# Performance work log

Measured on AMD Instinct MI355X. Metric: run time of the kernel, lower is better.

## Reference

```python
import jax, jax.numpy as jnp
import numpy as np

V, E, H, G, L, T, B = 32000, 1024, 16, 4, 8, 1024, 2
NKV = H // G          # kv heads = 4
D = E // H            # head dim = 64
BLOCK = 1024          # block_size
EPS = 1e-5


def setup_inputs() -> dict:
    key = jax.random.key(0)
    ks = jax.random.split(key, 12)
    f32 = jnp.float32
    return {
        "idx": jax.random.randint(ks[0], (B, T), 0, V),
        "tok_emb": jax.random.normal(ks[1], (V, E), f32),
        "pos_emb": jax.random.normal(ks[2], (BLOCK, E), f32),
        "q_proj": jax.random.normal(ks[3], (L, E, G, NKV, D), f32) / E**0.5,
        "kv_proj": jax.random.normal(ks[4], (L, 2, E, NKV, D), f32) / E**0.5,
        "out_proj": jax.random.normal(ks[5], (L, E, E), f32) / (D * H)**0.5,
        "fc_in": jax.random.normal(ks[6], (L, E, 4 * E), f32) / E**0.5,
        "fc_out": jax.random.normal(ks[7], (L, 4 * E, E), f32) / (4 * E)**0.5,
        "scale": jnp.ones((L, 2, E), f32),
        "out_scale": jnp.ones((E,), f32),
        "lm_head": jax.random.normal(ks[8], (E, V), f32) / E**0.5,
    }


def _ln(x, w):
    mu = jnp.mean(x, axis=-1, keepdims=True)
    var = jnp.var(x, axis=-1, keepdims=True)
    return (x - mu) * jax.lax.rsqrt(var + EPS) * w


def reference(idx, tok_emb, pos_emb, q_proj, kv_proj, out_proj, fc_in, fc_out, scale, out_scale, lm_head):
    x = tok_emb[idx] + pos_emb[:T]                         # [B,T,E]
    causal = jnp.tril(jnp.ones((T, T), bool))              # [T,T]
    neg_inf = jnp.float32(-jnp.inf)

    def layer(x, params):
        w_kv, w_q, w_out, fc1, fc2, lscale = params
        h = _ln(x, lscale[0])                              # pre-LN (note: residual uses h, matching source)
        q = jnp.einsum('btc,cgnd->bgntd', h, w_q)          # [B,G,NKV,T,D]
        kv = jnp.einsum('btc,scnd->sbntd', h, w_kv)        # [2,B,NKV,T,D]
        k, v = kv[0], kv[1]
        att = jnp.einsum('bgnqd,bnkd->bgnqk', q, k) * (D ** -0.5)
        att = jnp.where(causal, att, neg_inf)
        att = jax.nn.softmax(att, axis=-1)
        o = jnp.einsum('bgnqk,bnkd->bgnqd', att, v)        # [B,G,NKV,T,D]
        o = jnp.transpose(o, (0, 3, 1, 2, 4)).reshape(B, T, E)
        o = jnp.einsum('btc,cd->btd', o, w_out)
        h = h + o
        h = _ln(h, lscale[1])
        mlp = jax.nn.relu(jnp.einsum('btc,cf->btf', h, fc1))
        mlp = jnp.einsum('btf,fc->btc', mlp, fc2)
        return h + mlp, None

    x, _ = jax.lax.scan(layer, x, (kv_proj, q_proj, out_proj, fc_in, fc_out, scale))
    x = _ln(x, out_scale)
    logits = jnp.einsum('btc,cv->btv', x, lm_head)         # [B,T,V]
    return logits
```

## Files before the change

### kernel.cpp

```cpp
#include <hip/hip_runtime.h>
#include <hip/hip_bf16.h>

typedef __attribute__((ext_vector_type(8))) short bf16x8;
typedef __attribute__((ext_vector_type(4))) short bf16x4;
typedef __attribute__((ext_vector_type(4))) float f32x4;

#define LB __launch_bounds__(256)

__device__ __forceinline__ unsigned short f2b(float f) {
  __hip_bfloat16 h = __float2bfloat16(f);
  return __builtin_bit_cast(unsigned short, h);
}

#define GLDS(gp, lp)                                                        \
  __builtin_amdgcn_global_load_lds(                                         \
      (const __attribute__((address_space(1))) void*)(gp),                  \
      (__attribute__((address_space(3))) void*)(lp), 16, 0, 0)

__global__ LB void embed_kernel(const int* __restrict__ idx, const float* __restrict__ tok,
                                const float* __restrict__ pos, float* __restrict__ X) {
  const int m = blockIdx.x;
  const int t = m & 1023;
  const int token = idx[m];
  const int c = threadIdx.x * 4;
  const float4 a = *(const float4*)(tok + (size_t)token * 1024 + c);
  const float4 p = *(const float4*)(pos + (size_t)t * 1024 + c);
  float4 o; o.x = a.x + p.x; o.y = a.y + p.y; o.z = a.z + p.z; o.w = a.w + p.w;
  *(float4*)(X + (size_t)m * 1024 + c) = o;
}

template<bool WF32>
__global__ LB void ln_kernel(const float* __restrict__ X, const float* __restrict__ W,
                             float* __restrict__ Yf, unsigned short* __restrict__ Yb) {
  const int row = blockIdx.x;
  const float* xr = X + (size_t)row * 1024;
  const int c = threadIdx.x * 4;
  const float4 v = *(const float4*)(xr + c);
  float s = v.x + v.y + v.z + v.w;
  float q = v.x*v.x + v.y*v.y + v.z*v.z + v.w*v.w;
  #pragma unroll
  for (int d = 32; d > 0; d >>= 1) { s += __shfl_down(s, d); q += __shfl_down(q, d); }
  __shared__ float ss[4], sq[4];
  const int wid = threadIdx.x >> 6;
  if ((threadIdx.x & 63) == 0) { ss[wid] = s; sq[wid] = q; }
  __syncthreads();
  const float fs = ss[0] + ss[1] + ss[2] + ss[3];
  const float fq = sq[0] + sq[1] + sq[2] + sq[3];
  const float mean = fs * (1.0f / 1024.0f);
  const float var = fq * (1.0f / 1024.0f) - mean * mean;
  const float rstd = rsqrtf(var + 1e-5f);
  const float4 w = *(const float4*)(W + c);
  float4 o;
  o.x = (v.x - mean) * rstd * w.x; o.y = (v.y - mean) * rstd * w.y;
  o.z = (v.z - mean) * rstd * w.z; o.w = (v.w - mean) * rstd * w.w;
  if (WF32) *(float4*)(Yf + (size_t)row * 1024 + c) = o;
  unsigned long long pk = (unsigned long long)f2b(o.x)
      | ((unsigned long long)f2b(o.y) << 16)
      | ((unsigned long long)f2b(o.z) << 32)
      | ((unsigned long long)f2b(o.w) << 48);
  *(unsigned long long*)(Yb + (size_t)row * 1024 + c) = pk;
}

__device__ __forceinline__ void tr_body(const float* __restrict__ src,
                                        unsigned short* __restrict__ dst,
                                        int C, int rowOff, int ldDst, int bx, int by) {
  __shared__ float tile[32][33];
  const int c0 = bx * 32, r0 = by * 32;
  const int tx = threadIdx.x & 31, ty = threadIdx.x >> 5;
  #pragma unroll
  for (int u = 0; u < 4; ++u)
    tile[ty + u * 8][tx] = src[(size_t)(r0 + ty + u * 8) * C + c0 + tx];
  __syncthreads();
  const int ci = threadIdx.x >> 4;
  const int rp = threadIdx.x & 15;
  #pragma unroll
  for (int u = 0; u < 2; ++u) {
    const int c = ci + u * 16;
    unsigned int pk = (unsigned int)f2b(tile[rp * 2][c])
                    | ((unsigned int)f2b(tile[rp * 2 + 1][c]) << 16);
    *(unsigned int*)&dst[(size_t)(rowOff + c0 + c) * ldDst + r0 + rp * 2] = pk;
  }
}

__global__ LB void transpose_w(const float* __restrict__ src, unsigned short* __restrict__ dst,
                               int C, int rowOff, int ldDst) {
  tr_body(src, dst, C, rowOff, ldDst, blockIdx.x, blockIdx.y);
}

__global__ LB void transpose_all(const float* __restrict__ qp, const float* __restrict__ op,
                                 const float* __restrict__ kvp, unsigned short* __restrict__ dstQ,
                                 const float* __restrict__ f1, const float* __restrict__ f2,
                                 unsigned short* __restrict__ F1T, unsigned short* __restrict__ F2T) {
  int id = blockIdx.x;
  if (id < 2560) {
    const float* src; int C, rowOff, bx, by;
    if (id < 2048) {
      src = (id < 1024) ? qp : op;
      rowOff = (id < 1024) ? 0 : 1536;
      id &= 1023; C = 1024; bx = id & 31; by = id >> 5;
    } else {
      id -= 2048;
      src = (id < 256) ? kvp : (kvp + 1024 * 256);
      rowOff = (id < 256) ? 1024 : 1280;
      id &= 255; C = 256; bx = id & 7; by = id >> 3;
    }
    tr_body(src, dstQ, C, rowOff, 1024, bx, by);
  } else {
    id -= 2560;
    if (id < 4096) {
      tr_body(f1, F1T, 4096, 0, 1024, id & 127, id >> 7);
    } else {
      id -= 4096;
      tr_body(f2, F2T, 1024, 0, 4096, id & 31, id >> 5);
    }
  }
}

__global__ LB void attn_fused(const unsigned short* __restrict__ qkvb,
                              const unsigned short* __restrict__ vT,
                              unsigned short* __restrict__ ob) {
  const int qt = 15 - blockIdx.x, bh = blockIdx.y;
  const int b = bh >> 4, hh = bh & 15, n = hh & 3;
  const int tid = threadIdx.x, lane = tid & 63, w = tid >> 6;
  const int g = lane >> 4, c = lane & 15;
  const int q0w = qt * 64 + w * 16;
  const int qrow = q0w + c;

  __shared__ unsigned short lsK[2][64 * 64];
  __shared__ unsigned short lsV[2][64 * 64];
  __shared__ unsigned short lsP[4][16 * 64];
  unsigned short* Pw = lsP[w];

  bf16x8 qf[2];
  {
    const unsigned short* Qb = qkvb + (size_t)(b * 1024 + q0w) * 1536 + hh * 64;
    #pragma unroll
    for (int ks = 0; ks < 2; ++ks)
      qf[ks] = *(const bf16x8*)(Qb + (size_t)c * 1536 + ks * 32 + g * 8);
  }

  f32x4 accO[4] = {};
  float mr = -1e30f, lr = 0.0f;

  const int srow = tid >> 3;
  const int scol = ((tid & 7) ^ (srow & 7)) << 3;
  const unsigned short* gK = qkvb + (size_t)(b * 1024 + srow) * 1536 + 1024 + n * 64 + scol;
  const unsigned short* gV = vT + (size_t)((b * 4 + n) * 64 + srow) * 1024 + scol;

  GLDS(gK, &lsK[0][tid * 8]);
  GLDS(gK + (size_t)32 * 1536, &lsK[0][tid * 8 + 2048]);
  GLDS(gV, &lsV[0][tid * 8]);
  GLDS(gV + (size_t)32 * 1024, &lsV[0][tid * 8 + 2048]);
  __syncthreads();

  for (int kt = 0; kt <= qt; ++kt) {
    const int cur = kt & 1;
    if (kt < qt) {
      const size_t ko = (size_t)(kt + 1) * 64;
      GLDS(gK + ko * 1536, &lsK[cur ^ 1][tid * 8]);
      GLDS(gK + (ko + 32) * 1536, &lsK[cur ^ 1][tid * 8 + 2048]);
      GLDS(gV + ko, &lsV[cur ^ 1][tid * 8]);
      GLDS(gV + ko + (size_t)32 * 1024, &lsV[cur ^ 1][tid * 8 + 2048]);
    }
    const unsigned short* K_ = lsK[cur];
    const unsigned short* V_ = lsV[cur];
    const bool dg = (kt == qt);
    const int kb = kt * 64;

    f32x4 st[4] = {};
    #pragma unroll
    for (int ks = 0; ks < 2; ++ks) {
      const int col = (((ks * 4 + g) ^ (lane & 7)) << 3);
      bf16x8 kf[4];
      #pragma unroll
      for (int mi = 0; mi < 4; ++mi)
        kf[mi] = *(const bf16x8*)&K_[(mi * 16 + c) * 64 + col];
      #pragma unroll
      for (int mi = 0; mi < 4; ++mi)
        st[mi] = __builtin_amdgcn_mfma_f32_16x16x32_bf16(kf[mi], qf[ks], st[mi], 0, 0, 0);
    }

    float mx = mr;
    #pragma unroll
    for (int mi = 0; mi < 4; ++mi)
      #pragma unroll
      for (int j = 0; j < 4; ++j) {
        float v = st[mi][j] * 0.125f;
        if (dg && (kb + mi * 16 + g * 4 + j) > qrow) v = -1e30f;
        st[mi][j] = v;
        mx = fmaxf(mx, v);
      }
    mx = fmaxf(mx, __shfl_xor(mx, 16));
    mx = fmaxf(mx, __shfl_xor(mx, 32));
    const float al = __expf(mr - mx);
    float sum = 0.0f;
    #pragma unroll
    for (int mi = 0; mi < 4; ++mi) {
      bf16x4 pk;
      #pragma unroll
      for (int j = 0; j < 4; ++j) {
        const float e = __expf(st[mi][j] - mx);
        sum += e;
        pk[j] = (short)f2b(e);
      }
      *(bf16x4*)&Pw[c * 64 + ((mi * 16 + g * 4) ^ ((c & 7) << 3))] = pk;
    }
    sum += __shfl_xor(sum, 16);
    sum += __shfl_xor(sum, 32);
    lr = lr * al + sum;
    mr = mx;

    float aj[4];
    #pragma unroll
    for (int j = 0; j < 4; ++j) aj[j] = __shfl(al, g * 4 + j);
    #pragma unroll
    for (int dj = 0; dj < 4; ++dj)
      #pragma unroll
      for (int j = 0; j < 4; ++j) accO[dj][j] *= aj[j];

    #pragma unroll
    for (int ks = 0; ks < 2; ++ks) {
      const int col = (((ks * 4 + g) ^ (c & 7)) << 3);
      const bf16x8 pa = *(const bf16x8*)&Pw[c * 64 + col];
      bf16x8 vf[4];
      #pragma unroll
      for (int dj = 0; dj < 4; ++dj)
        vf[dj] = *(const bf16x8*)&V_[(dj * 16 + c) * 64 + col];
      #pragma unroll
      for (int dj = 0; dj < 4; ++dj)
        accO[dj] = __builtin_amdgcn_mfma_f32_16x16x32_bf16(pa, vf[dj], accO[dj], 0, 0, 0);
    }
    __syncthreads();
  }

  const float linv = 1.0f / lr;
  float lj[4];
  #pragma unroll
  for (int j = 0; j < 4; ++j) lj[j] = __shfl(linv, g * 4 + j);
  unsigned short* obase = ob + (size_t)(b * 1024 + q0w) * 1024 + hh * 64;
  #pragma unroll
  for (int dj = 0; dj < 4; ++dj)
    #pragma unroll
    for (int j = 0; j < 4; ++j)
      obase[(size_t)(g * 4 + j) * 1024 + dj * 16 + c] = f2b(accO[dj][j] * lj[j]);
}

template<int BM, int BN, bool BF16OUT, bool RELU, bool RESID, bool WVT = false, bool DBUF = false>
__global__ LB void gemm_nt(const unsigned short* __restrict__ A, const unsigned short* __restrict__ Bt,
                           void* __restrict__ Cv, const float* __restrict__ Res,
                           unsigned short* __restrict__ vTo,
                           int K, int lda, int ldb, int ldc) {
  constexpr int BK = 64;
  constexpr int WM = BM / 2, WN = BN / 2;
  constexpr int FM = WM / 16, FN = WN / 16;
  constexpr int PA = BM / 32, PB = BN / 32;
  constexpr int NB = DBUF ? 2 : 1;
  int f = blockIdx.x + gridDim.x * blockIdx.y;
  const int nwg = gridDim.x * gridDim.y;
  if ((nwg & 7) == 0) f = (f & 7) * (nwg >> 3) + (f >> 3);
  const int bx = f % gridDim.x, by = f / gridDim.x;

  const int tid = threadIdx.x;
  const int lane = tid & 63, wid = tid >> 6;
  const int wr = wid >> 1, wc = wid & 1;
  const int m0 = bx * BM, n0 = by * BN;

  __shared__ unsigned short lsA[NB][BM * BK];
  __shared__ unsigned short lsB[NB][BN * BK];

  f32x4 acc[FM][FN] = {};

  const int srow = tid >> 3;
  const int scol = ((tid & 7) ^ (srow & 7)) << 3;
  const unsigned short* gA = A + (size_t)(m0 + srow) * lda + scol;
  const unsigned short* gB = Bt + (size_t)(n0 + srow) * ldb + scol;

  const int fr = lane & 15;
  const int j7 = lane & 7;
  const int g4 = lane >> 4;

  if (DBUF) {
    #pragma unroll
    for (int p = 0; p < PA; ++p) GLDS(gA + (size_t)(p * 32) * lda, &lsA[0][tid * 8 + p * 2048]);
    #pragma unroll
    for (int p = 0; p < PB; ++p) GLDS(gB + (size_t)(p * 32) * ldb, &lsB[0][tid * 8 + p * 2048]);
    __syncthreads();
  }

  for (int k0 = 0; k0 < K; k0 += BK) {
    int cur = 0;
    if (DBUF) {
      cur = (k0 >> 6) & 1;
      if (k0 + BK < K) {
        #pragma unroll
        for (int p = 0; p < PA; ++p)
          GLDS(gA + (size_t)(p * 32) * lda + k0 + BK, &lsA[cur ^ 1][tid * 8 + p * 2048]);
        #pragma unroll
        for (int p = 0; p < PB; ++p)
          GLDS(gB + (size_t)(p * 32) * ldb + k0 + BK, &lsB[cur ^ 1][tid * 8 + p * 2048]);
      }
    } else {
      if (k0) __syncthreads();
      #pragma unroll
      for (int p = 0; p < PA; ++p)
        GLDS(gA + (size_t)(p * 32) * lda + k0, &lsA[0][tid * 8 + p * 2048]);
      #pragma unroll
      for (int p = 0; p < PB; ++p)
        GLDS(gB + (size_t)(p * 32) * ldb + k0, &lsB[0][tid * 8 + p * 2048]);
      __syncthreads();
    }

    const unsigned short* LA = lsA[cur];
    const unsigned short* LBp = lsB[cur];
    #pragma unroll
    for (int ks = 0; ks < 2; ++ks) {
      const int col = (((ks * 4 + g4) ^ j7) << 3);
      bf16x8 af[FM], bfv[FN];
      #pragma unroll
      for (int mi = 0; mi < FM; ++mi)
        af[mi] = *(const bf16x8*)&LA[(wr * WM + mi * 16 + fr) * BK + col];
      #pragma unroll
      for (int nj = 0; nj < FN; ++nj)
        bfv[nj] = *(const bf16x8*)&LBp[(wc * WN + nj * 16 + fr) * BK + col];
      #pragma unroll
      for (int mi = 0; mi < FM; ++mi)
        #pragma unroll
        for (int nj = 0; nj < FN; ++nj)
          acc[mi][nj] = __builtin_amdgcn_mfma_f32_16x16x32_bf16(af[mi], bfv[nj], acc[mi][nj], 0, 0, 0);
    }
    if (DBUF) __syncthreads();
  }

  const int r0 = (lane >> 4) * 4, c0 = lane & 15;
  #pragma unroll
  for (int mi = 0; mi < FM; ++mi) {
    #pragma unroll
    for (int nj = 0; nj < FN; ++nj) {
      const int c = n0 + wc * WN + nj * 16 + c0;
      const int rb = m0 + wr * WM + mi * 16 + r0;
      unsigned short us[4];
      #pragma unroll
      for (int j = 0; j < 4; ++j) {
        const int r = rb + j;
        float v = acc[mi][nj][j];
        if (RELU) v = fmaxf(v, 0.0f);
        if (RESID) v += Res[(size_t)r * ldc + c];
        const size_t o = (size_t)r * ldc + c;
        if (BF16OUT) { us[j] = f2b(v); ((unsigned short*)Cv)[o] = us[j]; }
        else ((float*)Cv)[o] = v;
      }
      if (WVT && c >= 1280) {
        const int bb = rb >> 10, t0 = rb & 1023;
        bf16x4 pk;
        #pragma unroll
        for (int j = 0; j < 4; ++j) pk[j] = (short)us[j];
        *(bf16x4*)&vTo[((size_t)(bb * 256 + (c - 1280))) * 1024 + t0] = pk;
      }
    }
  }
}

extern "C" void kernel_launch(void* const* d_in, const int* in_sizes, int n_in,
                              void* d_out, int out_size, void* d_ws, size_t ws_size,
                              hipStream_t stream) {
  (void)in_sizes; (void)n_in; (void)out_size;
  const int*   idx      = (const int*)d_in[0];
  const float* tok_emb  = (const float*)d_in[1];
  const float* pos_emb  = (const float*)d_in[2];
  const float* q_proj   = (const float*)d_in[3];
  const float* kv_proj  = (const float*)d_in[4];
  const float* out_proj = (const float*)d_in[5];
  const float* fc_in    = (const float*)d_in[6];
  const float* fc_out   = (const float*)d_in[7];
  const float* scale    = (const float*)d_in[8];
  const float* out_scl  = (const float*)d_in[9];
  const float* lm_head  = (const float*)d_in[10];
  float* out = (float*)d_out;

  char* ws = (char*)d_ws;
  size_t off = 0;
  auto alloc = [&](size_t bytes) -> void* {
    void* p = ws + off;
    off += (bytes + 255) & ~(size_t)255;
    return p;
  };
  unsigned short* WqkvT = (unsigned short*)alloc((size_t)2560 * 1024 * 2);
  unsigned short* WoT   = WqkvT + (size_t)1536 * 1024;
  unsigned short* F1T   = (unsigned short*)alloc((size_t)4096 * 1024 * 2);
  unsigned short* F2T   = (unsigned short*)alloc((size_t)1024 * 4096 * 2);
  float*  xbuf  = (float*)alloc((size_t)2048 * 1024 * 4);
  float*  hbuf  = (float*)alloc((size_t)2048 * 1024 * 4);
  float*  h2buf = (float*)alloc((size_t)2048 * 1024 * 4);
  unsigned short* actb  = (unsigned short*)alloc((size_t)2048 * 1024 * 2);
  unsigned short* qkvb  = (unsigned short*)alloc((size_t)2048 * 1536 * 2);
  unsigned short* vT    = (unsigned short*)alloc((size_t)2 * 256 * 1024 * 2);
  unsigned short* LmT   = (unsigned short*)alloc((size_t)32000 * 1024 * 2);
  unsigned short* ob    = (unsigned short*)alloc((size_t)2048 * 1024 * 2);
  unsigned short* m1    = (unsigned short*)alloc((size_t)2048 * 4096 * 2);
  if (off > ws_size) return;

  const dim3 thr(256);

  embed_kernel<<<dim3(2048), thr, 0, stream>>>(idx, tok_emb, pos_emb, xbuf);

  for (int l = 0; l < 8; ++l) {
    const float* qp  = q_proj + (size_t)l * 1024 * 1024;
    const float* op  = out_proj + (size_t)l * 1024 * 1024;
    const float* kvp = kv_proj + (size_t)l * 2 * 1024 * 256;
    transpose_all<<<dim3(10752), thr, 0, stream>>>(
        qp, op, kvp, WqkvT,
        fc_in + (size_t)l * 1024 * 4096, fc_out + (size_t)l * 4096 * 1024, F1T, F2T);

    const float* w1 = scale + (size_t)l * 2048;
    const float* w2 = w1 + 1024;

    ln_kernel<true><<<dim3(2048), thr, 0, stream>>>(xbuf, w1, hbuf, actb);
    gemm_nt<128, 64, true, false, false, true, true><<<dim3(16, 24), thr, 0, stream>>>(
        actb, WqkvT, qkvb, nullptr, vT, 1024, 1024, 1024, 1536);
    attn_fused<<<dim3(16, 32), thr, 0, stream>>>(qkvb, vT, ob);
    gemm_nt<128, 64, false, false, true, false, true><<<dim3(16, 16), thr, 0, stream>>>(
        ob, WoT, xbuf, hbuf, nullptr, 1024, 1024, 1024, 1024);
    ln_kernel<true><<<dim3(2048), thr, 0, stream>>>(xbuf, w2, h2buf, actb);
    gemm_nt<128, 128, true, true, false, false, true><<<dim3(16, 32), thr, 0, stream>>>(
        actb, F1T, m1, nullptr, nullptr, 1024, 1024, 1024, 4096);
    gemm_nt<128, 64, false, false, true, false, true><<<dim3(16, 16), thr, 0, stream>>>(
        m1, F2T, xbuf, h2buf, nullptr, 4096, 4096, 4096, 1024);
  }

  transpose_w<<<dim3(1000, 32), thr, 0, stream>>>(lm_head, LmT, 32000, 0, 1024);
  ln_kernel<false><<<dim3(2048), thr, 0, stream>>>(xbuf, out_scl, nullptr, actb);
  gemm_nt<128, 128, false, false, false><<<dim3(16, 250), thr, 0, stream>>>(
      actb, LmT, out, nullptr, nullptr, 1024, 1024, 1024, 32000);
}
```

Measured before the change: 1.536 ms.

## Add 256x256 double-buffered 8-wave GEMM for the LM head projection

Replaces the 128x128 LM-head GEMM with a new 512-thread kernel that computes 256x256 output tiles. It double-buffers XOR-swizzled LDS tiles filled by direct global-to-LDS loads, issues the next tile's loads interleaved across four quadrant sub-steps, raises wave priority around the MFMA bursts, and remaps workgroup IDs for locality. The goal is more data reuse per loaded byte and better overlap of memory traffic with matrix math on the largest GEMM. In exchange it uses 128 KB of LDS and many accumulator registers, which limits occupancy, and it needs careful manual vmcnt and barrier ordering.

```diff
diff --git a/kernel.cpp b/kernel.cpp
--- a/kernel.cpp
+++ b/kernel.cpp
@@ -16,6 +16,9 @@
   __builtin_amdgcn_global_load_lds(                                         \
       (const __attribute__((address_space(1))) void*)(gp),                  \
       (__attribute__((address_space(3))) void*)(lp), 16, 0, 0)
+
+#define WAITV(n) asm volatile("s_waitcnt vmcnt(" #n ")" ::: "memory")
+#define SBAR() do { __builtin_amdgcn_s_barrier(); asm volatile("" ::: "memory"); } while (0)
 
 __global__ LB void embed_kernel(const int* __restrict__ idx, const float* __restrict__ tok,
                                 const float* __restrict__ pos, float* __restrict__ X) {
@@ -355,6 +358,112 @@
         #pragma unroll
         for (int j = 0; j < 4; ++j) pk[j] = (short)us[j];
         *(bf16x4*)&vTo[((size_t)(bb * 256 + (c - 1280))) * 1024 + t0] = pk;
+      }
+    }
+  }
+}
+
+__global__ __launch_bounds__(512) void gemm_big(const unsigned short* __restrict__ A,
+                                                const unsigned short* __restrict__ Bt,
+                                                float* __restrict__ C,
+                                                int K, int lda, int ldb, int ldc) {
+  int f = blockIdx.x + gridDim.x * blockIdx.y;
+  const int nwg = gridDim.x * gridDim.y;
+  f = (f & 7) * (nwg >> 3) + (f >> 3);
+  const int bx = f % gridDim.x, by = f / gridDim.x;
+  const int m0 = bx * 256, n0 = by * 256;
+
+  const int tid = threadIdx.x;
+  const int lane = tid & 63, wid = tid >> 6;
+  const int wr = wid >> 2, wc = wid & 3;
+  const int fr = lane & 15, g4 = lane >> 4, j7 = lane & 7;
+
+  __shared__ unsigned short lsA[2][256 * 64];
+  __shared__ unsigned short lsB[2][256 * 64];
+
+  f32x4 acc[8][4] = {};
+
+  const int srow = tid >> 3;
+  const int scol = ((tid & 7) ^ (srow & 7)) << 3;
+  const unsigned short* gA = A + (size_t)(m0 + srow) * lda + scol;
+  const unsigned short* gB = Bt + (size_t)(n0 + srow) * ldb + scol;
+
+  const int nt = K >> 6;
+
+  GLDS(gB + (size_t)(0 * 64) * ldb, &lsB[0][tid * 8 + 0 * 4096]);
+  GLDS(gB + (size_t)(1 * 64) * ldb, &lsB[0][tid * 8 + 1 * 4096]);
+  GLDS(gB + (size_t)(2 * 64) * ldb, &lsB[0][tid * 8 + 2 * 4096]);
+  GLDS(gB + (size_t)(3 * 64) * ldb, &lsB[0][tid * 8 + 3 * 4096]);
+  GLDS(gA + (size_t)(0 * 64) * lda, &lsA[0][tid * 8 + 0 * 4096]);
+  GLDS(gA + (size_t)(2 * 64) * lda, &lsA[0][tid * 8 + 2 * 4096]);
+  GLDS(gA + (size_t)(1 * 64) * lda, &lsA[0][tid * 8 + 1 * 4096]);
+  GLDS(gA + (size_t)(3 * 64) * lda, &lsA[0][tid * 8 + 3 * 4096]);
+
+  for (int t = 0; t < nt; ++t) {
+    const int cur = t & 1;
+    const bool pref = (t + 1) < nt;
+    const int k1 = (t + 1) << 6;
+    const unsigned short* TA = lsA[cur];
+    const unsigned short* TB = lsB[cur];
+    unsigned short* nA = &lsA[cur ^ 1][tid * 8];
+    unsigned short* nB = &lsB[cur ^ 1][tid * 8];
+
+    WAITV(2);
+    SBAR();
+
+    #pragma unroll
+    for (int q = 0; q < 4; ++q) {
+      const int qm = q >> 1, qn = q & 1;
+      bf16x8 af[2][4], bf[2][2];
+      #pragma unroll
+      for (int ks = 0; ks < 2; ++ks) {
+        const int col = (((ks * 4 + g4) ^ j7) << 3);
+        #pragma unroll
+        for (int mi = 0; mi < 4; ++mi)
+          af[ks][mi] = *(const bf16x8*)&TA[(wr * 128 + qm * 64 + mi * 16 + fr) * 64 + col];
+        #pragma unroll
+        for (int nj = 0; nj < 2; ++nj)
+          bf[ks][nj] = *(const bf16x8*)&TB[(wc * 64 + (qn * 2 + nj) * 16 + fr) * 64 + col];
+      }
+      if (pref) {
+        if (q == 0) { GLDS(gB + (size_t)(0 * 64) * ldb + k1, nB + 0 * 4096);
+                      GLDS(gB + (size_t)(1 * 64) * ldb + k1, nB + 1 * 4096); }
+        else if (q == 1) { GLDS(gB + (size_t)(2 * 64) * ldb + k1, nB + 2 * 4096);
+                           GLDS(gB + (size_t)(3 * 64) * ldb + k1, nB + 3 * 4096); }
+        else if (q == 2) { GLDS(gA + (size_t)(0 * 64) * lda + k1, nA + 0 * 4096);
+                           GLDS(gA + (size_t)(2 * 64) * lda + k1, nA + 2 * 4096); }
+        else { GLDS(gA + (size_t)(1 * 64) * lda + k1, nA + 1 * 4096);
+               GLDS(gA + (size_t)(3 * 64) * lda + k1, nA + 3 * 4096); }
+      }
+      SBAR();
+      __builtin_amdgcn_s_setprio(1);
+      #pragma unroll
+      for (int ks = 0; ks < 2; ++ks)
+        #pragma unroll
+        for (int mi = 0; mi < 4; ++mi)
+          #pragma unroll
+          for (int nj = 0; nj < 2; ++nj)
+            acc[qm * 4 + mi][qn * 2 + nj] = __builtin_amdgcn_mfma_f32_16x16x32_bf16(
+                af[ks][mi], bf[ks][nj], acc[qm * 4 + mi][qn * 2 + nj], 0, 0, 0);
+      __builtin_amdgcn_s_setprio(0);
+      SBAR();
+      if (q == 1) {
+        if (pref) WAITV(4);
+        else      WAITV(0);
+        SBAR();
+      }
+    }
+  }
+
+  #pragma unroll
+  for (int mi = 0; mi < 8; ++mi) {
+    #pragma unroll
+    for (int nj = 0; nj < 4; ++nj) {
+      const int cc = n0 + wc * 64 + nj * 16 + fr;
+      #pragma unroll
+      for (int j = 0; j < 4; ++j) {
+        const int rr = m0 + wr * 128 + mi * 16 + g4 * 4 + j;
+        C[(size_t)rr * ldc + cc] = acc[mi][nj][j];
       }
     }
   }
@@ -429,6 +538,5 @@
 
   transpose_w<<<dim3(1000, 32), thr, 0, stream>>>(lm_head, LmT, 32000, 0, 1024);
   ln_kernel<false><<<dim3(2048), thr, 0, stream>>>(xbuf, out_scl, nullptr, actb);
-  gemm_nt<128, 128, false, false, false><<<dim3(16, 250), thr, 0, stream>>>(
-      actb, LmT, out, nullptr, nullptr, 1024, 1024, 1024, 32000);
-}
+  gemm_big<<<dim3(8, 125), dim3(512), 0, stream>>>(actb, LmT, out, 1024, 1024, 1024, 32000);
+}
```

After: 1.551 ms. Within noise of the previous version (+0.9%).
